# Kernel tuning notes

Measured on AMD Instinct MI355X. Metric: run time of the kernel, lower is better.

The kernel has to match this reference:

```python
import jax, jax.numpy as jnp
from jax import lax
import numpy as np

C = 256       # residual_channels == skip_channels
B = 4
T = 4096
LATENT = 128
NB = 4        # n_blocks
NL = 10       # n_layers
ENC_DILS = tuple(2 ** i for i in range(NL)) * NB   # 40 encoder blocks
DEC_DILS = tuple(2 ** i for i in range(NL))        # 10 decoder blocks


def causal_conv(x, W, b, d):
    # x: [B, Cin, T], W: [Cout, Cin, k], left-pad by (k-1)*d for causality
    pad = (W.shape[-1] - 1) * d
    y = lax.conv_general_dilated(x, W, (1,), [(pad, 0)], rhs_dilation=(d,),
                                 dimension_numbers=('NCH', 'OIH', 'NCH'))
    return y + b[None, :, None]


def gated_block(h, Wf, bf, Wg, bg, Wr, br, Ws, bs, d):
    f = jnp.tanh(causal_conv(h, Wf, bf, d))
    g = jax.nn.sigmoid(causal_conv(h, Wg, bg, d))
    out = f * g
    res = jnp.einsum('oc,bct->bot', Wr, out) + br[None, :, None] + h
    skip = jnp.einsum('oc,bct->bot', Ws, out) + bs[None, :, None]
    return res, skip


def setup_inputs() -> dict:
    key = jax.random.key(0)
    ks = jax.random.split(key, 24)
    s = 0.05
    nE = NB * NL
    d = {}
    d['x'] = jax.random.normal(ks[0], (B, 1, T), jnp.float32)
    d['eps'] = jax.random.normal(ks[1], (B, LATENT), jnp.float32)
    d['enc_in_W'] = jax.random.normal(ks[2], (C, 1, 2)) * s
    d['enc_in_b'] = jnp.zeros((C,), jnp.float32)
    d['enc_Wf'] = jax.random.normal(ks[3], (nE, C, C, 2)) * s
    d['enc_bf'] = jnp.zeros((nE, C), jnp.float32)
    d['enc_Wg'] = jax.random.normal(ks[4], (nE, C, C, 2)) * s
    d['enc_bg'] = jnp.zeros((nE, C), jnp.float32)
    d['enc_Wr'] = jax.random.normal(ks[5], (nE, C, C)) * s
    d['enc_br'] = jnp.zeros((nE, C), jnp.float32)
    d['enc_Ws'] = jax.random.normal(ks[6], (nE, C, C)) * s
    d['enc_bs'] = jnp.zeros((nE, C), jnp.float32)
    d['fc_mu_W'] = jax.random.normal(ks[7], (LATENT, C)) * s
    d['fc_mu_b'] = jnp.zeros((LATENT,), jnp.float32)
    d['fc_lv_W'] = jax.random.normal(ks[8], (LATENT, C)) * s
    d['fc_lv_b'] = jnp.zeros((LATENT,), jnp.float32)
    d['dec_in_W'] = jax.random.normal(ks[9], (C, LATENT)) * s
    d['dec_in_b'] = jnp.zeros((C,), jnp.float32)
    d['dec_Wf'] = jax.random.normal(ks[10], (NL, C, C, 2)) * s
    d['dec_bf'] = jnp.zeros((NL, C), jnp.float32)
    d['dec_Wg'] = jax.random.normal(ks[11], (NL, C, C, 2)) * s
    d['dec_bg'] = jnp.zeros((NL, C), jnp.float32)
    d['dec_Wr'] = jax.random.normal(ks[12], (NL, C, C)) * s
    d['dec_br'] = jnp.zeros((NL, C), jnp.float32)
    d['out_W'] = jax.random.normal(ks[13], (1, C)) * s
    d['out_b'] = jnp.zeros((1,), jnp.float32)
    return d


def _forward(x, eps, enc_in_W, enc_in_b, enc_Wf, enc_bf, enc_Wg, enc_bg,
             enc_Wr, enc_br, enc_Ws, enc_bs, fc_mu_W, fc_mu_b, fc_lv_W, fc_lv_b,
             dec_in_W, dec_in_b, dec_Wf, dec_bf, dec_Wg, dec_bg, dec_Wr, dec_br,
             out_W, out_b):
    # --- encode ---
    h = causal_conv(x, enc_in_W, enc_in_b, 1)
    skip_sum = jnp.zeros((h.shape[0], C, h.shape[2]), h.dtype)
    for i, dil in enumerate(ENC_DILS):
        h, skip = gated_block(h, enc_Wf[i], enc_bf[i], enc_Wg[i], enc_bg[i],
                              enc_Wr[i], enc_br[i], enc_Ws[i], enc_bs[i], dil)
        skip_sum = skip_sum + skip
    pooled = skip_sum.mean(axis=-1)                      # [B, C]
    mu = pooled @ fc_mu_W.T + fc_mu_b                    # [B, LATENT]
    logvar = pooled @ fc_lv_W.T + fc_lv_b
    # --- reparameterize ---
    z = mu + eps * jnp.exp(0.5 * logvar)
    # --- decode (length-1 sequence) ---
    h2 = (jnp.einsum('ol,bl->bo', dec_in_W, z) + dec_in_b)[:, :, None]  # [B, C, 1]
    for i, dil in enumerate(DEC_DILS):
        f = jnp.tanh(causal_conv(h2, dec_Wf[i], dec_bf[i], dil))
        g = jax.nn.sigmoid(causal_conv(h2, dec_Wg[i], dec_bg[i], dil))
        out = f * g
        h2 = jnp.einsum('oc,bct->bot', dec_Wr[i], out) + dec_br[i][None, :, None] + h2
    y = jnp.einsum('oc,bct->bot', out_W, h2) + out_b[None, :, None]     # [B, 1, 1]
    return (y, mu, logvar)


def reference(x, eps, enc_in_W, enc_in_b, enc_Wf, enc_bf, enc_Wg, enc_bg,
              enc_Wr, enc_br, enc_Ws, enc_bs, fc_mu_W, fc_mu_b, fc_lv_W, fc_lv_b,
              dec_in_W, dec_in_b, dec_Wf, dec_bf, dec_Wg, dec_bg, dec_Wr, dec_br,
              out_W, out_b):
    return _forward(x, eps, enc_in_W, enc_in_b, enc_Wf, enc_bf, enc_Wg, enc_bg,
                    enc_Wr, enc_br, enc_Ws, enc_bs, fc_mu_W, fc_mu_b, fc_lv_W, fc_lv_b,
                    dec_in_W, dec_in_b, dec_Wf, dec_bf, dec_Wg, dec_bg, dec_Wr, dec_br,
                    out_W, out_b)
```

## Files before the change

kernel.cpp:

```cpp
#include <hip/hip_runtime.h>

typedef unsigned short u16;
typedef __attribute__((ext_vector_type(8))) __bf16 bf16x8;
typedef __attribute__((ext_vector_type(4))) float f32x4;

constexpr int C = 256;
constexpr int T = 4096;
constexpr int B = 4;
constexpr int NENC = 40;
constexpr int NDEC = 10;
constexpr int TILE = 64;

__device__ __forceinline__ float bf2f(u16 v) {
  union { unsigned u; float f; } x;
  x.u = ((unsigned)v) << 16;
  return x.f;
}
__device__ __forceinline__ u16 f2bf(float f) {
  union { float ff; unsigned u; } x;
  x.ff = f;
  unsigned r = x.u + 0x7fffu + ((x.u >> 16) & 1u);
  return (u16)(r >> 16);
}
__device__ __forceinline__ int swz(int row, int col) {
  int g = ((row & 7) ^ (row >> 3)) & 7;
  return row * 512 + (col ^ (g << 3));
}

typedef __attribute__((address_space(1))) const unsigned int* gp1_t;
typedef __attribute__((address_space(3))) unsigned int* lp3_t;
__device__ __forceinline__ void gl_lds16(const u16* g, u16* l) {
  __builtin_amdgcn_global_load_lds((gp1_t)(const void*)g, (lp3_t)(void*)l, 16, 0, 0);
}

__global__ void k_pack1(const float* __restrict__ Wf, const float* __restrict__ Wg,
                        u16* __restrict__ penc1, int total) {
  int p = blockIdx.x * 256 + threadIdx.x;
  if (p >= total) return;
  int lane = p & 63;
  int s = (p >> 6) & 3;
  int c = (p >> 8) & 15;
  int wv = (p >> 12) & 7;
  int layer = p >> 15;
  int co = wv * 32 + (s & 1) * 16 + (lane & 15);
  int k = c * 32 + (lane >> 4) * 8;
  const float* src = (s >= 2 ? Wg : Wf) + ((size_t)layer * C + co) * 512 + k;
  u16* dst = penc1 + (size_t)p * 8;
#pragma unroll
  for (int r = 0; r < 8; ++r) dst[r] = f2bf(src[r]);
}

__global__ void k_pack2(const float* __restrict__ Wr, u16* __restrict__ penc2, int total) {
  int p = blockIdx.x * 256 + threadIdx.x;
  if (p >= total) return;
  int lane = p & 63;
  int s = (p >> 6) & 1;
  int c = (p >> 7) & 7;
  int wv = (p >> 10) & 7;
  int layer = p >> 13;
  int co = wv * 32 + s * 16 + (lane & 15);
  int k = c * 32 + (lane >> 4) * 8;
  const float* src = Wr + ((size_t)layer * C + co) * 256 + k;
  u16* dst = penc2 + (size_t)p * 8;
#pragma unroll
  for (int r = 0; r < 8; ++r) dst[r] = f2bf(src[r]);
}

__global__ void k_packd(const float* __restrict__ dWf, const float* __restrict__ dWg,
                        const float* __restrict__ dWr, const float* __restrict__ dinW,
                        u16* __restrict__ pdfg, u16* __restrict__ pdr,
                        u16* __restrict__ tdin) {
  int p = blockIdx.x * 256 + threadIdx.x;
  if (p < 163840) {
    int lane = p & 63;
    int s = (p >> 6) & 1;
    int c = (p >> 7) & 7;
    int wv = (p >> 10) & 15;
    int layer = p >> 14;
    int co = wv * 16 + (lane & 15);
    int k = c * 32 + (lane >> 4) * 8;
    const float* src = (s ? dWg : dWf) + (((size_t)(layer * C + co)) * C + k) * 2 + 1;
    u16* dst = pdfg + (size_t)p * 8;
#pragma unroll
    for (int r = 0; r < 8; ++r) dst[r] = f2bf(src[2 * r]);
  } else if (p < 245760) {
    int q = p - 163840;
    int lane = q & 63;
    int c = (q >> 6) & 7;
    int wv = (q >> 9) & 15;
    int layer = q >> 13;
    int co = wv * 16 + (lane & 15);
    int k = c * 32 + (lane >> 4) * 8;
    const float* src = dWr + ((size_t)(layer * C + co)) * C + k;
    u16* dst = pdr + (size_t)q * 8;
#pragma unroll
    for (int r = 0; r < 8; ++r) dst[r] = f2bf(src[r]);
  } else if (p < 249856) {
    int u = p - 245760;
#pragma unroll
    for (int r = 0; r < 8; ++r) tdin[u * 8 + r] = f2bf(dinW[u * 8 + r]);
  }
}

__global__ void k_zero(float* __restrict__ p, int n) {
  int i = blockIdx.x * 256 + threadIdx.x;
  if (i < n) p[i] = 0.f;
}

__global__ void k_input(const float* __restrict__ x, const float* __restrict__ W,
                        const float* __restrict__ bin, float* __restrict__ h) {
  int idx = blockIdx.x * 256 + threadIdx.x;
  int t = idx & (T - 1);
  int c = (idx >> 12) & (C - 1);
  int b = idx >> 20;
  float xv = x[b * T + t];
  float xp = (t > 0) ? x[b * T + t - 1] : 0.f;
  h[idx] = W[2 * c] * xp + W[2 * c + 1] * xv + bin[c];
}

__global__ __launch_bounds__(512, 2) void k_enc(
    const float* __restrict__ hin, float* __restrict__ hout, float* __restrict__ rowsum_l,
    const u16* __restrict__ pw1, const float* __restrict__ bfb,
    const float* __restrict__ bgb,
    const u16* __restrict__ pw2, const float* __restrict__ brb,
    int dil) {
  extern __shared__ __align__(16) u16 smem[];
  u16* wb = smem + 64 * 512;
  const int tid = threadIdx.x;
  const int wave = tid >> 6;
  const int lane = tid & 63;
  const int ncol = lane & 15;
  const int quad = lane >> 4;
  const int wg = blockIdx.x;
  const int b = wg >> 6;
  const int t0 = (wg & 63) * TILE;
  const float* hb = hin + b * C * T;

  const int co0 = wave * 32;
  const int kq = quad * 8;
  const int off1 = (wg >> 3) & 15;
  const int off2 = (wg >> 3) & 7;
  const u16* b1 = pw1 + wave * 32768 + lane * 8;
  const u16* b2 = pw2 + wave * 8192 + lane * 8;
  u16* wreg0 = wb + wave * 2048;
  u16* wreg1 = wb + 16384 + wave * 2048;
  const int aoff = lane * 8;

#pragma unroll
  for (int cc = 0; cc < 2; ++cc) {
    u16* ld = cc ? wreg1 : wreg0;
    const u16* gs = b1 + ((off1 + cc) & 15) * 2048;
    gl_lds16(gs, ld);
    gl_lds16(gs + 512, ld + 512);
    gl_lds16(gs + 1024, ld + 1024);
    gl_lds16(gs + 1536, ld + 1536);
  }

  const int n4 = tid & 15;
  const int cib = tid >> 4;
  float4 v[16];
  const bool al4 = ((dil & 3) == 0);
  if (t0 >= dil) {
#pragma unroll
    for (int it2 = 0; it2 < 16; ++it2) {
      int ci = (cib + it2 * 32) & 255;
      int tap = it2 >> 3;
      int tb = t0 + n4 * 4 - (tap ? 0 : dil);
      const float* p = hb + ci * T + tb;
      if (tap || al4) {
        v[it2] = *(const float4*)p;
      } else {
        v[it2].x = p[0]; v[it2].y = p[1]; v[it2].z = p[2]; v[it2].w = p[3];
      }
    }
  } else {
#pragma unroll
    for (int it2 = 0; it2 < 16; ++it2) {
      int ci = (cib + it2 * 32) & 255;
      int tap = it2 >> 3;
      int tb = t0 + n4 * 4 - (tap ? 0 : dil);
      const float* p = hb + ci * T + tb;
      if (tap) {
        v[it2] = *(const float4*)p;
      } else {
        v[it2].x = (tb + 0 >= 0) ? p[0] : 0.f;
        v[it2].y = (tb + 1 >= 0) ? p[1] : 0.f;
        v[it2].z = (tb + 2 >= 0) ? p[2] : 0.f;
        v[it2].w = (tb + 3 >= 0) ? p[3] : 0.f;
      }
    }
  }
#pragma unroll
  for (int it2 = 0; it2 < 8; ++it2) {
    int ci = (cib + it2 * 32) & 255;
    const float* p0 = (const float*)&v[it2];
    const float* p1 = (const float*)&v[it2 + 8];
#pragma unroll
    for (int r = 0; r < 4; ++r) {
      unsigned w32 = (unsigned)f2bf(p0[r]) | ((unsigned)f2bf(p1[r]) << 16);
      *(unsigned*)(&smem[swz(n4 * 4 + r, 2 * ci)]) = w32;
    }
  }
  __syncthreads();

  f32x4 acc[4][4];
#pragma unroll
  for (int m = 0; m < 4; ++m)
#pragma unroll
    for (int nt = 0; nt < 4; ++nt)
      acc[m][nt] = (f32x4){0.f, 0.f, 0.f, 0.f};

#pragma unroll
  for (int c = 0; c < 16; ++c) {
    if (c < 15) asm volatile("s_waitcnt vmcnt(4)" ::: "memory");
    else        asm volatile("s_waitcnt vmcnt(0)" ::: "memory");
    const u16* wr_ = (c & 1) ? wreg1 : wreg0;
    bf16x8 af0 = *(const bf16x8*)(wr_ + aoff);
    bf16x8 af1 = *(const bf16x8*)(wr_ + 512 + aoff);
    bf16x8 af2 = *(const bf16x8*)(wr_ + 1024 + aoff);
    bf16x8 af3 = *(const bf16x8*)(wr_ + 1536 + aoff);
    const int kk = ((c + off1) & 15) * 32 + kq;
    bf16x8 bfr[4];
#pragma unroll
    for (int nt = 0; nt < 4; ++nt)
      bfr[nt] = *(const bf16x8*)(&smem[swz(nt * 16 + ncol, kk)]);
#pragma unroll
    for (int nt = 0; nt < 4; ++nt) {
      acc[0][nt] = __builtin_amdgcn_mfma_f32_16x16x32_bf16(af0, bfr[nt], acc[0][nt], 0, 0, 0);
      acc[1][nt] = __builtin_amdgcn_mfma_f32_16x16x32_bf16(af1, bfr[nt], acc[1][nt], 0, 0, 0);
      acc[2][nt] = __builtin_amdgcn_mfma_f32_16x16x32_bf16(af2, bfr[nt], acc[2][nt], 0, 0, 0);
      acc[3][nt] = __builtin_amdgcn_mfma_f32_16x16x32_bf16(af3, bfr[nt], acc[3][nt], 0, 0, 0);
    }
    if (c + 2 < 16) {
      asm volatile("s_waitcnt lgkmcnt(0)" ::: "memory");
      u16* ld = (c & 1) ? wreg1 : wreg0;
      const u16* gs = b1 + ((c + 2 + off1) & 15) * 2048;
      gl_lds16(gs, ld);
      gl_lds16(gs + 512, ld + 512);
      gl_lds16(gs + 1024, ld + 1024);
      gl_lds16(gs + 1536, ld + 1536);
    }
  }

#pragma unroll
  for (int cc = 0; cc < 2; ++cc) {
    u16* ld = cc ? wreg1 : wreg0;
    const u16* gs = b2 + ((off2 + cc) & 7) * 1024;
    gl_lds16(gs, ld);
    gl_lds16(gs + 512, ld + 512);
  }
  __syncthreads();

  float* rsb = rowsum_l + b * C;
#pragma unroll
  for (int j = 0; j < 2; ++j) {
    const int cob = co0 + j * 16 + quad * 4;
    float bfv[4], bgv[4], rs[4];
#pragma unroll
    for (int r = 0; r < 4; ++r) {
      bfv[r] = bfb[cob + r];
      bgv[r] = bgb[cob + r];
      rs[r] = 0.f;
    }
#pragma unroll
    for (int nt = 0; nt < 4; ++nt) {
      const int n = nt * 16 + ncol;
      u16 pk[4];
#pragma unroll
      for (int r = 0; r < 4; ++r) {
        float fv = acc[j][nt][r] + bfv[r];
        float gv = acc[2 + j][nt][r] + bgv[r];
        float th = 1.f - 2.f / (__expf(2.f * fv) + 1.f);
        float sg = 1.f / (1.f + __expf(-gv));
        float o = th * sg;
        rs[r] += o;
        pk[r] = f2bf(o);
      }
      uint2 w;
      w.x = (unsigned)pk[0] | ((unsigned)pk[1] << 16);
      w.y = (unsigned)pk[2] | ((unsigned)pk[3] << 16);
      *(uint2*)(&smem[swz(n, cob)]) = w;
    }
#pragma unroll
    for (int r = 0; r < 4; ++r) {
      float s = rs[r];
      s += __shfl_xor(s, 1);
      s += __shfl_xor(s, 2);
      s += __shfl_xor(s, 4);
      s += __shfl_xor(s, 8);
      if (ncol == 0) atomicAdd(&rsb[cob + r], s);
    }
  }
  __syncthreads();

  f32x4 acc2[2][4];
#pragma unroll
  for (int m = 0; m < 2; ++m)
#pragma unroll
    for (int nt = 0; nt < 4; ++nt)
      acc2[m][nt] = (f32x4){0.f, 0.f, 0.f, 0.f};

#pragma unroll
  for (int c = 0; c < 8; ++c) {
    if (c < 7) asm volatile("s_waitcnt vmcnt(2)" ::: "memory");
    else       asm volatile("s_waitcnt vmcnt(0)" ::: "memory");
    const u16* wr_ = (c & 1) ? wreg1 : wreg0;
    bf16x8 af0 = *(const bf16x8*)(wr_ + aoff);
    bf16x8 af1 = *(const bf16x8*)(wr_ + 512 + aoff);
    const int kk = ((c + off2) & 7) * 32 + kq;
    bf16x8 bfr[4];
#pragma unroll
    for (int nt = 0; nt < 4; ++nt)
      bfr[nt] = *(const bf16x8*)(&smem[swz(nt * 16 + ncol, kk)]);
#pragma unroll
    for (int nt = 0; nt < 4; ++nt) {
      acc2[0][nt] = __builtin_amdgcn_mfma_f32_16x16x32_bf16(af0, bfr[nt], acc2[0][nt], 0, 0, 0);
      acc2[1][nt] = __builtin_amdgcn_mfma_f32_16x16x32_bf16(af1, bfr[nt], acc2[1][nt], 0, 0, 0);
    }
    if (c + 2 < 8) {
      asm volatile("s_waitcnt lgkmcnt(0)" ::: "memory");
      u16* ld = (c & 1) ? wreg1 : wreg0;
      const u16* gs = b2 + ((c + 2 + off2) & 7) * 1024;
      gl_lds16(gs, ld);
      gl_lds16(gs + 512, ld + 512);
    }
  }
  __syncthreads();

  float* fb = (float*)smem;
#pragma unroll
  for (int m = 0; m < 2; ++m) {
    const int cob = co0 + m * 16 + quad * 4;
#pragma unroll
    for (int nt = 0; nt < 4; ++nt) {
      const int t = nt * 16 + ncol;
#pragma unroll
      for (int r = 0; r < 4; ++r)
        fb[(cob + r) * 66 + t] = acc2[m][nt][r] + brb[cob + r];
    }
  }
  __syncthreads();
  float* ho = hout + b * C * T;
#pragma unroll
  for (int it2 = 0; it2 < 8; ++it2) {
    const int ci = cib + it2 * 32;
    const float* fr = fb + ci * 66 + n4 * 4;
    float4 o;
    o.x = fr[0] + v[it2 + 8].x;
    o.y = fr[1] + v[it2 + 8].y;
    o.z = fr[2] + v[it2 + 8].z;
    o.w = fr[3] + v[it2 + 8].w;
    *(float4*)(ho + ci * T + t0 + n4 * 4) = o;
  }
}

__global__ __launch_bounds__(256) void k_skip(
    const float* __restrict__ encWs, const float* __restrict__ encbs,
    const float* __restrict__ rowsum, float* __restrict__ pooled) {
  __shared__ float rs[B][C];
  const int l = blockIdx.x;
  const int co = threadIdx.x;
  for (int i = co; i < B * C; i += 256) rs[i >> 8][i & 255] = rowsum[l * B * C + i];
  __syncthreads();
  const float* Wrow = encWs + (size_t)l * C * C + co * C;
  float bs = encbs[l * C + co] * (float)T;
  float d[B] = {0.f, 0.f, 0.f, 0.f};
  for (int ci = 0; ci < C; ci += 4) {
    float4 w = *(const float4*)(Wrow + ci);
#pragma unroll
    for (int b = 0; b < B; ++b)
      d[b] += w.x * rs[b][ci] + w.y * rs[b][ci + 1] + w.z * rs[b][ci + 2] + w.w * rs[b][ci + 3];
  }
#pragma unroll
  for (int b = 0; b < B; ++b) atomicAdd(&pooled[b * C + co], d[b] + bs);
}

__global__ __launch_bounds__(256) void k_fc(
    const float* __restrict__ pooled,
    const float* __restrict__ muW, const float* __restrict__ mub,
    const float* __restrict__ lvW, const float* __restrict__ lvb,
    float* __restrict__ mlbuf, float* __restrict__ dout) {
  __shared__ float pm[B * C];
  const int tid = threadIdx.x;
  for (int i = tid; i < B * C; i += 256) pm[i] = pooled[i] * (1.f / (float)T);
  __syncthreads();
  const int waveG = blockIdx.x * 4 + (tid >> 6);
  const int lane = tid & 63;
  for (int j = 0; j < 16; ++j) {
    int d = waveG * 16 + j;
    int b = d >> 8, r = d & 255, which = r >> 7, l = r & 127;
    const float* Wrow = (which ? lvW : muW) + l * C;
    const float* p = pm + b * C;
    float s = Wrow[lane] * p[lane] + Wrow[lane + 64] * p[lane + 64] +
              Wrow[lane + 128] * p[lane + 128] + Wrow[lane + 192] * p[lane + 192];
#pragma unroll
    for (int off = 32; off; off >>= 1) s += __shfl_xor(s, off);
    if (lane == 0) {
      float val = s + (which ? lvb[l] : mub[l]);
      mlbuf[which * 512 + b * 128 + l] = val;
      dout[4 + which * 512 + b * 128 + l] = val;
    }
  }
}

__global__ __launch_bounds__(1024, 1) void k_dec(
    const float* __restrict__ mlbuf, const float* __restrict__ eps,
    const u16* __restrict__ tdin, const float* __restrict__ dinb,
    const u16* __restrict__ pdfg, const float* __restrict__ dbf,
    const float* __restrict__ dbg,
    const u16* __restrict__ pdr, const float* __restrict__ dbr,
    const float* __restrict__ outW, const float* __restrict__ outb,
    float* __restrict__ dout) {
  extern __shared__ __align__(16) u16 dsm[];
  __shared__ __align__(16) u16 Ah[16][264];
  __shared__ __align__(16) u16 Ao[16][264];
  __shared__ float h2f[4][256];
  __shared__ float outred[4];
  const int tid = threadIdx.x;
  const int wave = tid >> 6;
  const int lane = tid & 63;
  const int ncol = lane & 15;
  const int quad = lane >> 4;
  const int kq = quad * 8;
  const int co = wave * 16 + ncol;
  u16* wreg = dsm + wave * 4096;

  bf16x8 tdw[4];
  {
    const u16* wp = tdin + co * 128;
#pragma unroll
    for (int it = 0; it < 4; ++it) tdw[it] = *(const bf16x8*)(wp + it * 32 + kq);
  }

  if (tid < 512) {
    int b = tid >> 7, l = tid & 127;
    float mu = mlbuf[b * 128 + l];
    float lv = mlbuf[512 + b * 128 + l];
    Ah[b][l] = f2bf(mu + eps[b * 128 + l] * expf(0.5f * lv));
  }
  if (tid < 4) outred[tid] = 0.f;
  __syncthreads();

  {
    f32x4 acch = (f32x4){0.f, 0.f, 0.f, 0.f};
#pragma unroll
    for (int it = 0; it < 4; ++it) {
      bf16x8 af = *(const bf16x8*)(&Ah[ncol][it * 32 + kq]);
      acch = __builtin_amdgcn_mfma_f32_16x16x32_bf16(af, tdw[it], acch, 0, 0, 0);
    }
    __syncthreads();
    if (quad == 0) {
      float bias = dinb[co];
#pragma unroll
      for (int r = 0; r < 4; ++r) {
        float hv = acch[r] + bias;
        h2f[r][co] = hv;
        Ah[r][co] = f2bf(hv);
      }
    }
  }
  {
    const u16* fb = pdfg + wave * 8192 + lane * 8;
#pragma unroll
    for (int cc = 0; cc < 4; ++cc) {
      gl_lds16(fb + cc * 1024, wreg + cc * 1024);
      gl_lds16(fb + cc * 1024 + 512, wreg + cc * 1024 + 512);
    }
  }
  __syncthreads();

  for (int i = 0; i < NDEC; ++i) {
    const u16* fb = pdfg + (i * 16 + wave) * 8192 + lane * 8;
    const u16* rb = pdr + (i * 16 + wave) * 4096 + lane * 8;

    f32x4 accf = (f32x4){0.f, 0.f, 0.f, 0.f};
    f32x4 accg = (f32x4){0.f, 0.f, 0.f, 0.f};
#pragma unroll
    for (int c = 0; c < 8; ++c) {
      if (c == 4) asm volatile("s_waitcnt vmcnt(6)" ::: "memory");
      else if (c == 5) asm volatile("s_waitcnt vmcnt(4)" ::: "memory");
      else if (c == 6) asm volatile("s_waitcnt vmcnt(2)" ::: "memory");
      else if (c == 7) asm volatile("s_waitcnt vmcnt(0)" ::: "memory");
      const u16* bufp = wreg + (c & 3) * 1024;
      bf16x8 bf_ = *(const bf16x8*)(bufp + lane * 8);
      bf16x8 bg_ = *(const bf16x8*)(bufp + 512 + lane * 8);
      bf16x8 af = *(const bf16x8*)(&Ah[ncol][c * 32 + kq]);
      accf = __builtin_amdgcn_mfma_f32_16x16x32_bf16(af, bf_, accf, 0, 0, 0);
      accg = __builtin_amdgcn_mfma_f32_16x16x32_bf16(af, bg_, accg, 0, 0, 0);
      if (c < 4) {
        asm volatile("s_waitcnt lgkmcnt(0)" ::: "memory");
        gl_lds16(fb + (c + 4) * 1024, wreg + (c & 3) * 1024);
        gl_lds16(fb + (c + 4) * 1024 + 512, wreg + (c & 3) * 1024 + 512);
      }
    }
    asm volatile("s_waitcnt lgkmcnt(0)" ::: "memory");
#pragma unroll
    for (int cc = 0; cc < 4; ++cc) gl_lds16(rb + cc * 512, wreg + cc * 1024);

    if (quad == 0) {
      float bfv = dbf[i * C + co];
      float bgv = dbg[i * C + co];
#pragma unroll
      for (int r = 0; r < 4; ++r) {
        float fv = accf[r] + bfv;
        float gv = accg[r] + bgv;
        float th = 1.f - 2.f / (__expf(2.f * fv) + 1.f);
        float sg = 1.f / (1.f + __expf(-gv));
        Ao[r][co] = f2bf(th * sg);
      }
    }
    __syncthreads();

    f32x4 accr = (f32x4){0.f, 0.f, 0.f, 0.f};
#pragma unroll
    for (int c = 0; c < 8; ++c) {
      if (c == 4) asm volatile("s_waitcnt vmcnt(3)" ::: "memory");
      else if (c == 5) asm volatile("s_waitcnt vmcnt(2)" ::: "memory");
      else if (c == 6) asm volatile("s_waitcnt vmcnt(1)" ::: "memory");
      else if (c == 7) asm volatile("s_waitcnt vmcnt(0)" ::: "memory");
      bf16x8 br_ = *(const bf16x8*)(wreg + (c & 3) * 1024 + lane * 8);
      bf16x8 af = *(const bf16x8*)(&Ao[ncol][c * 32 + kq]);
      accr = __builtin_amdgcn_mfma_f32_16x16x32_bf16(af, br_, accr, 0, 0, 0);
      if (c < 4) {
        asm volatile("s_waitcnt lgkmcnt(0)" ::: "memory");
        gl_lds16(rb + (c + 4) * 512, wreg + (c & 3) * 1024);
      }
    }
    if (i + 1 < NDEC) {
      const u16* nfb = pdfg + ((i + 1) * 16 + wave) * 8192 + lane * 8;
      asm volatile("s_waitcnt lgkmcnt(0)" ::: "memory");
#pragma unroll
      for (int cc = 0; cc < 4; ++cc) {
        gl_lds16(nfb + cc * 1024, wreg + cc * 1024);
        gl_lds16(nfb + cc * 1024 + 512, wreg + cc * 1024 + 512);
      }
    }
    if (quad == 0) {
      float brv = dbr[i * C + co];
#pragma unroll
      for (int r = 0; r < 4; ++r) {
        float hv = h2f[r][co] + accr[r] + brv;
        h2f[r][co] = hv;
        Ah[r][co] = f2bf(hv);
      }
    }
    __syncthreads();
  }

  {
    int b = tid >> 8, c = tid & 255;
    float val = outW[c] * h2f[b][c];
#pragma unroll
    for (int off = 32; off; off >>= 1) val += __shfl_xor(val, off);
    if (lane == 0) atomicAdd(&outred[b], val);
  }
  __syncthreads();
  if (tid < 4) dout[tid] = outred[tid] + outb[0];
}

extern "C" void kernel_launch(void* const* d_in, const int* in_sizes, int n_in,
                              void* d_out, int out_size, void* d_ws, size_t ws_size,
                              hipStream_t stream) {
  const float* x      = (const float*)d_in[0];
  const float* eps    = (const float*)d_in[1];
  const float* encinW = (const float*)d_in[2];
  const float* encinb = (const float*)d_in[3];
  const float* encWf  = (const float*)d_in[4];
  const float* encbf  = (const float*)d_in[5];
  const float* encWg  = (const float*)d_in[6];
  const float* encbg  = (const float*)d_in[7];
  const float* encWr  = (const float*)d_in[8];
  const float* encbr  = (const float*)d_in[9];
  const float* encWs  = (const float*)d_in[10];
  const float* encbs  = (const float*)d_in[11];
  const float* muW    = (const float*)d_in[12];
  const float* mub    = (const float*)d_in[13];
  const float* lvW    = (const float*)d_in[14];
  const float* lvb    = (const float*)d_in[15];
  const float* dinW   = (const float*)d_in[16];
  const float* dinb   = (const float*)d_in[17];
  const float* dWf    = (const float*)d_in[18];
  const float* dbf    = (const float*)d_in[19];
  const float* dWg    = (const float*)d_in[20];
  const float* dbg    = (const float*)d_in[21];
  const float* dWr    = (const float*)d_in[22];
  const float* dbr    = (const float*)d_in[23];
  const float* outW   = (const float*)d_in[24];
  const float* outb   = (const float*)d_in[25];
  float* dout = (float*)d_out;

  char* ws = (char*)d_ws;
  float* hA = (float*)ws;
  float* hB = hA + (size_t)B * C * T;
  float* pooled = hB + (size_t)B * C * T;
  float* mlbuf = pooled + B * C;
  float* rowsum = mlbuf + 1024;
  u16* penc1 = (u16*)(rowsum + NENC * B * C);
  u16* penc2 = penc1 + (size_t)10485760;
  u16* pdfg = penc2 + (size_t)2621440;
  u16* pdr = pdfg + (size_t)1310720;
  u16* tdin = pdr + (size_t)655360;

  (void)hipFuncSetAttribute(reinterpret_cast<const void*>(k_enc),
                            hipFuncAttributeMaxDynamicSharedMemorySize, 131072);
  (void)hipFuncSetAttribute(reinterpret_cast<const void*>(k_dec),
                            hipFuncAttributeMaxDynamicSharedMemorySize, 131072);

  k_pack1<<<(1310720 + 255) / 256, 256, 0, stream>>>(encWf, encWg, penc1, 1310720);
  k_pack2<<<(327680 + 255) / 256, 256, 0, stream>>>(encWr, penc2, 327680);
  k_packd<<<(249856 + 255) / 256, 256, 0, stream>>>(dWf, dWg, dWr, dinW, pdfg, pdr, tdin);

  const int nZ = B * C + 1024 + NENC * B * C;
  k_zero<<<(nZ + 255) / 256, 256, 0, stream>>>(pooled, nZ);
  k_input<<<(B * C * T) / 256, 256, 0, stream>>>(x, encinW, encinb, hA);

  for (int i = 0; i < NENC; ++i) {
    const int dil = 1 << (i % 10);
    const float* hi = (i & 1) ? hB : hA;
    float* ho = (i & 1) ? hA : hB;
    k_enc<<<256, 512, 131072, stream>>>(
        hi, ho, rowsum + (size_t)i * B * C,
        penc1 + (size_t)i * 262144, encbf + (size_t)i * C,
        encbg + (size_t)i * C,
        penc2 + (size_t)i * 65536, encbr + (size_t)i * C,
        dil);
  }

  k_skip<<<NENC, 256, 0, stream>>>(encWs, encbs, rowsum, pooled);
  k_fc<<<16, 256, 0, stream>>>(pooled, muW, mub, lvW, lvb, mlbuf, dout);
  k_dec<<<1, 1024, 131072, stream>>>(mlbuf, eps, tdin, dinb, pdfg, dbf, dbg,
                                     pdr, dbr, outW, outb, dout);
}
```

Baseline: 1.270 ms.

## Widen encoder time tile to 128 with per-tap staging; split decoder launch

The encoder kernel now processes 128 timesteps per workgroup instead of 64, using 128 workgroups. The input activations are staged one conv tap at a time into a half-width swizzled LDS buffer, and the packed gate weights are reordered tap-major to match. This doubles reuse of each streamed weight chunk across time columns, roughly halving weight traffic per layer. The costs are fewer workgroups than CUs, more accumulator registers, an extra mid-loop barrier, and re-reading the residual input from global memory. The single-block decoder is split into four launches that pass state through global memory, adding launch overhead for unclear benefit.

```diff
diff --git a/kernel.cpp b/kernel.cpp
--- a/kernel.cpp
+++ b/kernel.cpp
@@ -9,7 +9,6 @@
 constexpr int B = 4;
 constexpr int NENC = 40;
 constexpr int NDEC = 10;
-constexpr int TILE = 64;
 
 __device__ __forceinline__ float bf2f(u16 v) {
   union { unsigned u; float f; } x;
@@ -22,9 +21,9 @@
   unsigned r = x.u + 0x7fffu + ((x.u >> 16) & 1u);
   return (u16)(r >> 16);
 }
-__device__ __forceinline__ int swz(int row, int col) {
+__device__ __forceinline__ int swz2(int row, int col) {
   int g = ((row & 7) ^ (row >> 3)) & 7;
-  return row * 512 + (col ^ (g << 3));
+  return row * 256 + (col ^ (g << 3));
 }
 
 typedef __attribute__((address_space(1))) const unsigned int* gp1_t;
@@ -39,15 +38,16 @@
   if (p >= total) return;
   int lane = p & 63;
   int s = (p >> 6) & 3;
-  int c = (p >> 8) & 15;
-  int wv = (p >> 12) & 7;
+  int chunk = (p >> 8) & 7;
+  int wv = (p >> 11) & 7;
+  int tap = (p >> 14) & 1;
   int layer = p >> 15;
   int co = wv * 32 + (s & 1) * 16 + (lane & 15);
-  int k = c * 32 + (lane >> 4) * 8;
-  const float* src = (s >= 2 ? Wg : Wf) + ((size_t)layer * C + co) * 512 + k;
+  int ci = chunk * 32 + (lane >> 4) * 8;
+  const float* src = (s >= 2 ? Wg : Wf) + (((size_t)layer * C + co) * C + ci) * 2 + tap;
   u16* dst = penc1 + (size_t)p * 8;
 #pragma unroll
-  for (int r = 0; r < 8; ++r) dst[r] = f2bf(src[r]);
+  for (int r = 0; r < 8; ++r) dst[r] = f2bf(src[2 * r]);
 }
 
 __global__ void k_pack2(const float* __restrict__ Wr, u16* __restrict__ penc2, int total) {
@@ -118,6 +118,47 @@
   h[idx] = W[2 * c] * xp + W[2 * c + 1] * xv + bin[c];
 }
 
+__device__ __forceinline__ void stage_tap(const float* __restrict__ hb, u16* __restrict__ smem,
+                                          int t0, int dil, int tap, int tid) {
+  const int n5 = tid & 31;
+  const int cib = tid >> 5;
+  const int tb = t0 + n5 * 4 - (tap ? 0 : dil);
+  const bool safe = (tb >= 0);
+  const bool al4 = tap || ((dil & 3) == 0);
+#pragma unroll
+  for (int it2 = 0; it2 < 8; ++it2) {
+    int ci0 = cib * 16 + it2 * 2;
+    const float* p0 = hb + ci0 * T + tb;
+    const float* p1 = p0 + T;
+    float4 a, c;
+    if (safe) {
+      if (al4) {
+        a = *(const float4*)p0;
+        c = *(const float4*)p1;
+      } else {
+        a.x = p0[0]; a.y = p0[1]; a.z = p0[2]; a.w = p0[3];
+        c.x = p1[0]; c.y = p1[1]; c.z = p1[2]; c.w = p1[3];
+      }
+    } else {
+      a.x = (tb + 0 >= 0) ? p0[0] : 0.f;
+      a.y = (tb + 1 >= 0) ? p0[1] : 0.f;
+      a.z = (tb + 2 >= 0) ? p0[2] : 0.f;
+      a.w = (tb + 3 >= 0) ? p0[3] : 0.f;
+      c.x = (tb + 0 >= 0) ? p1[0] : 0.f;
+      c.y = (tb + 1 >= 0) ? p1[1] : 0.f;
+      c.z = (tb + 2 >= 0) ? p1[2] : 0.f;
+      c.w = (tb + 3 >= 0) ? p1[3] : 0.f;
+    }
+    const float* pa = (const float*)&a;
+    const float* pc = (const float*)&c;
+#pragma unroll
+    for (int r = 0; r < 4; ++r) {
+      unsigned w32 = (unsigned)f2bf(pa[r]) | ((unsigned)f2bf(pc[r]) << 16);
+      *(unsigned*)(&smem[swz2(n5 * 4 + r, ci0)]) = w32;
+    }
+  }
+}
+
 __global__ __launch_bounds__(512, 2) void k_enc(
     const float* __restrict__ hin, float* __restrict__ hout, float* __restrict__ rowsum_l,
     const u16* __restrict__ pw1, const float* __restrict__ bfb,
@@ -125,116 +166,75 @@
     const u16* __restrict__ pw2, const float* __restrict__ brb,
     int dil) {
   extern __shared__ __align__(16) u16 smem[];
-  u16* wb = smem + 64 * 512;
+  u16* wb = smem + 32768;
   const int tid = threadIdx.x;
   const int wave = tid >> 6;
   const int lane = tid & 63;
   const int ncol = lane & 15;
   const int quad = lane >> 4;
+  const int kq = quad * 8;
   const int wg = blockIdx.x;
-  const int b = wg >> 6;
-  const int t0 = (wg & 63) * TILE;
+  const int b = wg >> 5;
+  const int t0 = (wg & 31) * 128;
   const float* hb = hin + b * C * T;
 
   const int co0 = wave * 32;
-  const int kq = quad * 8;
-  const int off1 = (wg >> 3) & 15;
-  const int off2 = (wg >> 3) & 7;
-  const u16* b1 = pw1 + wave * 32768 + lane * 8;
-  const u16* b2 = pw2 + wave * 8192 + lane * 8;
-  u16* wreg0 = wb + wave * 2048;
-  u16* wreg1 = wb + 16384 + wave * 2048;
+  const u16* b1w = pw1 + wave * 16384 + lane * 8;
+  const u16* b2w = pw2 + wave * 8192 + lane * 8;
+  u16* wbuf0 = wb + wave * 2048;
+  u16* wbuf1 = wb + 16384 + wave * 2048;
   const int aoff = lane * 8;
 
 #pragma unroll
-  for (int cc = 0; cc < 2; ++cc) {
-    u16* ld = cc ? wreg1 : wreg0;
-    const u16* gs = b1 + ((off1 + cc) & 15) * 2048;
+  for (int q = 0; q < 2; ++q) {
+    u16* ld = q ? wbuf1 : wbuf0;
+    const u16* gs = b1w + q * 2048;
     gl_lds16(gs, ld);
     gl_lds16(gs + 512, ld + 512);
     gl_lds16(gs + 1024, ld + 1024);
     gl_lds16(gs + 1536, ld + 1536);
   }
-
-  const int n4 = tid & 15;
-  const int cib = tid >> 4;
-  float4 v[16];
-  const bool al4 = ((dil & 3) == 0);
-  if (t0 >= dil) {
-#pragma unroll
-    for (int it2 = 0; it2 < 16; ++it2) {
-      int ci = (cib + it2 * 32) & 255;
-      int tap = it2 >> 3;
-      int tb = t0 + n4 * 4 - (tap ? 0 : dil);
-      const float* p = hb + ci * T + tb;
-      if (tap || al4) {
-        v[it2] = *(const float4*)p;
-      } else {
-        v[it2].x = p[0]; v[it2].y = p[1]; v[it2].z = p[2]; v[it2].w = p[3];
-      }
-    }
-  } else {
-#pragma unroll
-    for (int it2 = 0; it2 < 16; ++it2) {
-      int ci = (cib + it2 * 32) & 255;
-      int tap = it2 >> 3;
-      int tb = t0 + n4 * 4 - (tap ? 0 : dil);
-      const float* p = hb + ci * T + tb;
-      if (tap) {
-        v[it2] = *(const float4*)p;
-      } else {
-        v[it2].x = (tb + 0 >= 0) ? p[0] : 0.f;
-        v[it2].y = (tb + 1 >= 0) ? p[1] : 0.f;
-        v[it2].z = (tb + 2 >= 0) ? p[2] : 0.f;
-        v[it2].w = (tb + 3 >= 0) ? p[3] : 0.f;
-      }
-    }
-  }
-#pragma unroll
-  for (int it2 = 0; it2 < 8; ++it2) {
-    int ci = (cib + it2 * 32) & 255;
-    const float* p0 = (const float*)&v[it2];
-    const float* p1 = (const float*)&v[it2 + 8];
-#pragma unroll
-    for (int r = 0; r < 4; ++r) {
-      unsigned w32 = (unsigned)f2bf(p0[r]) | ((unsigned)f2bf(p1[r]) << 16);
-      *(unsigned*)(&smem[swz(n4 * 4 + r, 2 * ci)]) = w32;
-    }
-  }
+  stage_tap(hb, smem, t0, dil, 0, tid);
   __syncthreads();
 
-  f32x4 acc[4][4];
+  f32x4 acc[4][8];
 #pragma unroll
   for (int m = 0; m < 4; ++m)
 #pragma unroll
-    for (int nt = 0; nt < 4; ++nt)
+    for (int nt = 0; nt < 8; ++nt)
       acc[m][nt] = (f32x4){0.f, 0.f, 0.f, 0.f};
 
 #pragma unroll
-  for (int c = 0; c < 16; ++c) {
-    if (c < 15) asm volatile("s_waitcnt vmcnt(4)" ::: "memory");
-    else        asm volatile("s_waitcnt vmcnt(0)" ::: "memory");
-    const u16* wr_ = (c & 1) ? wreg1 : wreg0;
+  for (int gc = 0; gc < 16; ++gc) {
+    if (gc == 8) {
+      __syncthreads();
+      stage_tap(hb, smem, t0, dil, 1, tid);
+      __syncthreads();
+    }
+    if (gc < 15) asm volatile("s_waitcnt vmcnt(4)" ::: "memory");
+    else         asm volatile("s_waitcnt vmcnt(0)" ::: "memory");
+    const u16* wr_ = (gc & 1) ? wbuf1 : wbuf0;
     bf16x8 af0 = *(const bf16x8*)(wr_ + aoff);
     bf16x8 af1 = *(const bf16x8*)(wr_ + 512 + aoff);
     bf16x8 af2 = *(const bf16x8*)(wr_ + 1024 + aoff);
     bf16x8 af3 = *(const bf16x8*)(wr_ + 1536 + aoff);
-    const int kk = ((c + off1) & 15) * 32 + kq;
-    bf16x8 bfr[4];
-#pragma unroll
-    for (int nt = 0; nt < 4; ++nt)
-      bfr[nt] = *(const bf16x8*)(&smem[swz(nt * 16 + ncol, kk)]);
-#pragma unroll
-    for (int nt = 0; nt < 4; ++nt) {
+    const int kk = (gc & 7) * 32 + kq;
+    bf16x8 bfr[8];
+#pragma unroll
+    for (int nt = 0; nt < 8; ++nt)
+      bfr[nt] = *(const bf16x8*)(&smem[swz2(nt * 16 + ncol, kk)]);
+#pragma unroll
+    for (int nt = 0; nt < 8; ++nt) {
       acc[0][nt] = __builtin_amdgcn_mfma_f32_16x16x32_bf16(af0, bfr[nt], acc[0][nt], 0, 0, 0);
       acc[1][nt] = __builtin_amdgcn_mfma_f32_16x16x32_bf16(af1, bfr[nt], acc[1][nt], 0, 0, 0);
       acc[2][nt] = __builtin_amdgcn_mfma_f32_16x16x32_bf16(af2, bfr[nt], acc[2][nt], 0, 0, 0);
       acc[3][nt] = __builtin_amdgcn_mfma_f32_16x16x32_bf16(af3, bfr[nt], acc[3][nt], 0, 0, 0);
     }
-    if (c + 2 < 16) {
+    if (gc + 2 < 16) {
       asm volatile("s_waitcnt lgkmcnt(0)" ::: "memory");
-      u16* ld = (c & 1) ? wreg1 : wreg0;
-      const u16* gs = b1 + ((c + 2 + off1) & 15) * 2048;
+      u16* ld = (gc & 1) ? wbuf1 : wbuf0;
+      const int nc = gc + 2;
+      const u16* gs = b1w + (nc >> 3) * 131072 + (nc & 7) * 2048;
       gl_lds16(gs, ld);
       gl_lds16(gs + 512, ld + 512);
       gl_lds16(gs + 1024, ld + 1024);
@@ -243,9 +243,9 @@
   }
 
 #pragma unroll
-  for (int cc = 0; cc < 2; ++cc) {
-    u16* ld = cc ? wreg1 : wreg0;
-    const u16* gs = b2 + ((off2 + cc) & 7) * 1024;
+  for (int q = 0; q < 2; ++q) {
+    u16* ld = q ? wbuf1 : wbuf0;
+    const u16* gs = b2w + q * 1024;
     gl_lds16(gs, ld);
     gl_lds16(gs + 512, ld + 512);
   }
@@ -263,8 +263,8 @@
       rs[r] = 0.f;
     }
 #pragma unroll
-    for (int nt = 0; nt < 4; ++nt) {
-      const int n = nt * 16 + ncol;
+    for (int nt = 0; nt < 8; ++nt) {
+      const int t = nt * 16 + ncol;
       u16 pk[4];
 #pragma unroll
       for (int r = 0; r < 4; ++r) {
@@ -279,7 +279,7 @@
       uint2 w;
       w.x = (unsigned)pk[0] | ((unsigned)pk[1] << 16);
       w.y = (unsigned)pk[2] | ((unsigned)pk[3] << 16);
-      *(uint2*)(&smem[swz(n, cob)]) = w;
+      *(uint2*)(&smem[swz2(t, cob)]) = w;
     }
 #pragma unroll
     for (int r = 0; r < 4; ++r) {
@@ -293,64 +293,72 @@
   }
   __syncthreads();
 
-  f32x4 acc2[2][4];
+  f32x4 acc2[2][8];
 #pragma unroll
   for (int m = 0; m < 2; ++m)
 #pragma unroll
-    for (int nt = 0; nt < 4; ++nt)
+    for (int nt = 0; nt < 8; ++nt)
       acc2[m][nt] = (f32x4){0.f, 0.f, 0.f, 0.f};
 
 #pragma unroll
   for (int c = 0; c < 8; ++c) {
     if (c < 7) asm volatile("s_waitcnt vmcnt(2)" ::: "memory");
     else       asm volatile("s_waitcnt vmcnt(0)" ::: "memory");
-    const u16* wr_ = (c & 1) ? wreg1 : wreg0;
+    const u16* wr_ = (c & 1) ? wbuf1 : wbuf0;
     bf16x8 af0 = *(const bf16x8*)(wr_ + aoff);
     bf16x8 af1 = *(const bf16x8*)(wr_ + 512 + aoff);
-    const int kk = ((c + off2) & 7) * 32 + kq;
-    bf16x8 bfr[4];
-#pragma unroll
-    for (int nt = 0; nt < 4; ++nt)
-      bfr[nt] = *(const bf16x8*)(&smem[swz(nt * 16 + ncol, kk)]);
-#pragma unroll
-    for (int nt = 0; nt < 4; ++nt) {
+    const int kk = c * 32 + kq;
+    bf16x8 bfr[8];
+#pragma unroll
+    for (int nt = 0; nt < 8; ++nt)
+      bfr[nt] = *(const bf16x8*)(&smem[swz2(nt * 16 + ncol, kk)]);
+#pragma unroll
+    for (int nt = 0; nt < 8; ++nt) {
       acc2[0][nt] = __builtin_amdgcn_mfma_f32_16x16x32_bf16(af0, bfr[nt], acc2[0][nt], 0, 0, 0);
       acc2[1][nt] = __builtin_amdgcn_mfma_f32_16x16x32_bf16(af1, bfr[nt], acc2[1][nt], 0, 0, 0);
     }
     if (c + 2 < 8) {
       asm volatile("s_waitcnt lgkmcnt(0)" ::: "memory");
-      u16* ld = (c & 1) ? wreg1 : wreg0;
-      const u16* gs = b2 + ((c + 2 + off2) & 7) * 1024;
+      u16* ld = (c & 1) ? wbuf1 : wbuf0;
+      const u16* gs = b2w + (c + 2) * 1024;
       gl_lds16(gs, ld);
       gl_lds16(gs + 512, ld + 512);
     }
   }
   __syncthreads();
 
-  float* fb = (float*)smem;
-#pragma unroll
-  for (int m = 0; m < 2; ++m) {
-    const int cob = co0 + m * 16 + quad * 4;
-#pragma unroll
-    for (int nt = 0; nt < 4; ++nt) {
-      const int t = nt * 16 + ncol;
-#pragma unroll
-      for (int r = 0; r < 4; ++r)
-        fb[(cob + r) * 66 + t] = acc2[m][nt][r] + brb[cob + r];
-    }
-  }
-  __syncthreads();
+  float* fbuf = (float*)smem;
   float* ho = hout + b * C * T;
-#pragma unroll
-  for (int it2 = 0; it2 < 8; ++it2) {
-    const int ci = cib + it2 * 32;
-    const float* fr = fb + ci * 66 + n4 * 4;
-    float4 o;
-    o.x = fr[0] + v[it2 + 8].x;
-    o.y = fr[1] + v[it2 + 8].y;
-    o.z = fr[2] + v[it2 + 8].z;
-    o.w = fr[3] + v[it2 + 8].w;
-    *(float4*)(ho + ci * T + t0 + n4 * 4) = o;
+  const int n4 = tid & 15;
+  const int cib2 = tid >> 4;
+#pragma unroll
+  for (int h = 0; h < 2; ++h) {
+    if (h) __syncthreads();
+#pragma unroll
+    for (int j = 0; j < 2; ++j) {
+      const int cob = co0 + j * 16 + quad * 4;
+#pragma unroll
+      for (int nt = 4 * h; nt < 4 * h + 4; ++nt) {
+        const int tl = nt * 16 + ncol - 64 * h;
+#pragma unroll
+        for (int r = 0; r < 4; ++r)
+          fbuf[(cob + r) * 66 + tl] = acc2[j][nt][r] + brb[cob + r];
+      }
+    }
+    __syncthreads();
+#pragma unroll
+    for (int it2 = 0; it2 < 8; ++it2) {
+      const int ci = cib2 + it2 * 32;
+      const int tg = t0 + h * 64 + n4 * 4;
+      float4 hv = *(const float4*)(hb + ci * T + tg);
+      const float* fr = fbuf + ci * 66 + n4 * 4;
+      float4 o;
+      o.x = fr[0] + hv.x;
+      o.y = fr[1] + hv.y;
+      o.z = fr[2] + hv.z;
+      o.w = fr[3] + hv.w;
+      *(float4*)(ho + ci * T + tg) = o;
+    }
   }
 }
 
@@ -410,7 +418,8 @@
     const float* __restrict__ dbg,
     const u16* __restrict__ pdr, const float* __restrict__ dbr,
     const float* __restrict__ outW, const float* __restrict__ outb,
-    float* __restrict__ dout) {
+    float* __restrict__ gstate, float* __restrict__ dout,
+    int l0, int l1, int head, int tail) {
   extern __shared__ __align__(16) u16 dsm[];
   __shared__ __align__(16) u16 Ah[16][264];
   __shared__ __align__(16) u16 Ao[16][264];
@@ -425,23 +434,20 @@
   const int co = wave * 16 + ncol;
   u16* wreg = dsm + wave * 4096;
 
-  bf16x8 tdw[4];
-  {
-    const u16* wp = tdin + co * 128;
-#pragma unroll
-    for (int it = 0; it < 4; ++it) tdw[it] = *(const bf16x8*)(wp + it * 32 + kq);
-  }
-
-  if (tid < 512) {
-    int b = tid >> 7, l = tid & 127;
-    float mu = mlbuf[b * 128 + l];
-    float lv = mlbuf[512 + b * 128 + l];
-    Ah[b][l] = f2bf(mu + eps[b * 128 + l] * expf(0.5f * lv));
-  }
-  if (tid < 4) outred[tid] = 0.f;
-  __syncthreads();
-
-  {
+  if (head) {
+    bf16x8 tdw[4];
+    {
+      const u16* wp = tdin + co * 128;
+#pragma unroll
+      for (int it = 0; it < 4; ++it) tdw[it] = *(const bf16x8*)(wp + it * 32 + kq);
+    }
+    if (tid < 512) {
+      int b = tid >> 7, l = tid & 127;
+      float mu = mlbuf[b * 128 + l];
+      float lv = mlbuf[512 + b * 128 + l];
+      Ah[b][l] = f2bf(mu + eps[b * 128 + l] * expf(0.5f * lv));
+    }
+    __syncthreads();
     f32x4 acch = (f32x4){0.f, 0.f, 0.f, 0.f};
 #pragma unroll
     for (int it = 0; it < 4; ++it) {
@@ -458,9 +464,15 @@
         Ah[r][co] = f2bf(hv);
       }
     }
-  }
+  } else {
+    float hv = gstate[tid & 1023];
+    int b = (tid >> 8) & 3, c = tid & 255;
+    h2f[b][c] = hv;
+    Ah[b][c] = f2bf(hv);
+  }
+  if (tid < 4) outred[tid] = 0.f;
   {
-    const u16* fb = pdfg + wave * 8192 + lane * 8;
+    const u16* fb = pdfg + (l0 * 16 + wave) * 8192 + lane * 8;
 #pragma unroll
     for (int cc = 0; cc < 4; ++cc) {
       gl_lds16(fb + cc * 1024, wreg + cc * 1024);
@@ -469,7 +481,7 @@
   }
   __syncthreads();
 
-  for (int i = 0; i < NDEC; ++i) {
+  for (int i = l0; i < l1; ++i) {
     const u16* fb = pdfg + (i * 16 + wave) * 8192 + lane * 8;
     const u16* rb = pdr + (i * 16 + wave) * 4096 + lane * 8;
 
@@ -526,7 +538,7 @@
         gl_lds16(rb + (c + 4) * 512, wreg + (c & 3) * 1024);
       }
     }
-    if (i + 1 < NDEC) {
+    if (i + 1 < l1) {
       const u16* nfb = pdfg + ((i + 1) * 16 + wave) * 8192 + lane * 8;
       asm volatile("s_waitcnt lgkmcnt(0)" ::: "memory");
 #pragma unroll
@@ -547,15 +559,17 @@
     __syncthreads();
   }
 
-  {
+  if (tail) {
     int b = tid >> 8, c = tid & 255;
     float val = outW[c] * h2f[b][c];
 #pragma unroll
     for (int off = 32; off; off >>= 1) val += __shfl_xor(val, off);
     if (lane == 0) atomicAdd(&outred[b], val);
-  }
-  __syncthreads();
-  if (tid < 4) dout[tid] = outred[tid] + outb[0];
+    __syncthreads();
+    if (tid < 4) dout[tid] = outred[tid] + outb[0];
+  } else {
+    gstate[tid & 1023] = h2f[(tid >> 8) & 3][tid & 255];
+  }
 }
 
 extern "C" void kernel_launch(void* const* d_in, const int* in_sizes, int n_in,
@@ -595,7 +609,8 @@
   float* pooled = hB + (size_t)B * C * T;
   float* mlbuf = pooled + B * C;
   float* rowsum = mlbuf + 1024;
-  u16* penc1 = (u16*)(rowsum + NENC * B * C);
+  float* gstate = rowsum + NENC * B * C;
+  u16* penc1 = (u16*)(gstate + 1024);
   u16* penc2 = penc1 + (size_t)10485760;
   u16* pdfg = penc2 + (size_t)2621440;
   u16* pdr = pdfg + (size_t)1310720;
@@ -618,7 +633,7 @@
     const int dil = 1 << (i % 10);
     const float* hi = (i & 1) ? hB : hA;
     float* ho = (i & 1) ? hA : hB;
-    k_enc<<<256, 512, 131072, stream>>>(
+    k_enc<<<128, 512, 131072, stream>>>(
         hi, ho, rowsum + (size_t)i * B * C,
         penc1 + (size_t)i * 262144, encbf + (size_t)i * C,
         encbg + (size_t)i * C,
@@ -629,5 +644,11 @@
   k_skip<<<NENC, 256, 0, stream>>>(encWs, encbs, rowsum, pooled);
   k_fc<<<16, 256, 0, stream>>>(pooled, muW, mub, lvW, lvb, mlbuf, dout);
   k_dec<<<1, 1024, 131072, stream>>>(mlbuf, eps, tdin, dinb, pdfg, dbf, dbg,
-                                     pdr, dbr, outW, outb, dout);
-}
+                                     pdr, dbr, outW, outb, gstate, dout, 0, 3, 1, 0);
+  k_dec<<<1, 1024, 131072, stream>>>(mlbuf, eps, tdin, dinb, pdfg, dbf, dbg,
+                                     pdr, dbr, outW, outb, gstate, dout, 3, 6, 0, 0);
+  k_dec<<<1, 1024, 131072, stream>>>(mlbuf, eps, tdin, dinb, pdfg, dbf, dbg,
+                                     pdr, dbr, outW, outb, gstate, dout, 6, 8, 0, 0);
+  k_dec<<<1, 1024, 131072, stream>>>(mlbuf, eps, tdin, dinb, pdfg, dbf, dbg,
+                                     pdr, dbr, outW, outb, gstate, dout, 8, 10, 0, 1);
+}
```

Result: slower. 2.595 ms (+104.3%).
